# Kernel optimization log

Hardware: AMD Instinct MI355X
Metric: run time of the kernel (lower is better)

## Reference

```python
import jax, jax.numpy as jnp
import numpy as np

HID = 10


def _lstm_cell(xt, h, c, W_ih, W_hh, b_ih, b_hh):
    # PyTorch LSTMCell: gates ordered (i, f, g, o)
    gates = xt @ W_ih.T + b_ih + h @ W_hh.T + b_hh  # [B, 4*HID]
    i, f, g, o = jnp.split(gates, 4, axis=-1)
    c_new = jax.nn.sigmoid(f) * c + jax.nn.sigmoid(i) * jnp.tanh(g)
    h_new = jax.nn.sigmoid(o) * jnp.tanh(c_new)
    return h_new, c_new


def setup_inputs() -> dict:
    key = jax.random.key(0)
    ks = jax.random.split(key, 12)
    B, T = 2048, 1024
    s = 0.1
    return {
        "x": jax.random.normal(ks[0], (B, T), dtype=jnp.float32),
        "W_ih1": jax.random.normal(ks[1], (4 * HID, 1), dtype=jnp.float32) * s,
        "W_hh1": jax.random.normal(ks[2], (4 * HID, HID), dtype=jnp.float32) * s,
        "b_ih1": jax.random.normal(ks[3], (4 * HID,), dtype=jnp.float32) * s,
        "b_hh1": jax.random.normal(ks[4], (4 * HID,), dtype=jnp.float32) * s,
        "W_ih2": jax.random.normal(ks[5], (4 * HID, HID), dtype=jnp.float32) * s,
        "W_hh2": jax.random.normal(ks[6], (4 * HID, HID), dtype=jnp.float32) * s,
        "b_ih2": jax.random.normal(ks[7], (4 * HID,), dtype=jnp.float32) * s,
        "b_ih2b": None,  # placeholder removed below
        "b_hh2": jax.random.normal(ks[8], (4 * HID,), dtype=jnp.float32) * s,
        "W_lin": jax.random.normal(ks[9], (1, HID), dtype=jnp.float32) * s,
        "b_lin": jax.random.normal(ks[10], (1,), dtype=jnp.float32) * s,
        "future": 64,
    } if False else {
        "x": jax.random.normal(ks[0], (B, T), dtype=jnp.float32),
        "W_ih1": jax.random.normal(ks[1], (4 * HID, 1), dtype=jnp.float32) * s,
        "W_hh1": jax.random.normal(ks[2], (4 * HID, HID), dtype=jnp.float32) * s,
        "b_ih1": jax.random.normal(ks[3], (4 * HID,), dtype=jnp.float32) * s,
        "b_hh1": jax.random.normal(ks[4], (4 * HID,), dtype=jnp.float32) * s,
        "W_ih2": jax.random.normal(ks[5], (4 * HID, HID), dtype=jnp.float32) * s,
        "W_hh2": jax.random.normal(ks[6], (4 * HID, HID), dtype=jnp.float32) * s,
        "b_ih2": jax.random.normal(ks[7], (4 * HID,), dtype=jnp.float32) * s,
        "b_hh2": jax.random.normal(ks[8], (4 * HID,), dtype=jnp.float32) * s,
        "W_lin": jax.random.normal(ks[9], (1, HID), dtype=jnp.float32) * s,
        "b_lin": jax.random.normal(ks[10], (1,), dtype=jnp.float32) * s,
        "future": 64,
    }


def _forward(x, W_ih1, W_hh1, b_ih1, b_hh1, W_ih2, W_hh2, b_ih2, b_hh2,
             W_lin, b_lin, future):
    B = x.shape[0]
    z = jnp.zeros((B, HID), dtype=x.dtype)
    state0 = (z, z, z, z)  # h1, c1, h2, c2

    def step(state, xt):
        h1, c1, h2, c2 = state
        h1, c1 = _lstm_cell(xt, h1, c1, W_ih1, W_hh1, b_ih1, b_hh1)
        h2, c2 = _lstm_cell(h1, h2, c2, W_ih2, W_hh2, b_ih2, b_hh2)
        y = h2 @ W_lin.T + b_lin  # [B, 1]
        return (h1, c1, h2, c2), y

    xs = x.T[:, :, None]  # [T, B, 1]
    state, ys = jax.lax.scan(step, state0, xs)  # ys: [T, B, 1]
    outs = ys[:, :, 0].T  # [B, T]

    if future > 0:
        last = ys[-1]  # [B, 1]

        def fstep(carry, _):
            state, y = carry
            state, y_new = step(state, y)
            return (state, y_new), y_new

        (_, _), fys = jax.lax.scan(fstep, (state, last), None, length=future)
        outs = jnp.concatenate([outs, fys[:, :, 0].T], axis=1)
    return outs  # [B, T + future]


def reference(x, W_ih1, W_hh1, b_ih1, b_hh1, W_ih2, W_hh2, b_ih2, b_hh2,
              W_lin, b_lin, future):
    return _forward(x, W_ih1, W_hh1, b_ih1, b_hh1, W_ih2, W_hh2, b_ih2,
                    b_hh2, W_lin, b_lin, future)
```

## Files before the change

### kernel.cpp

```cpp
#include <hip/hip_runtime.h>


#define NB 512
#define TMAIN 1024
#define HID 10
#define KCH 16
#define NCH (TMAIN / KCH)

typedef float v2f __attribute__((ext_vector_type(2)));
typedef float v4f __attribute__((ext_vector_type(4)));

#define PIN2(v) asm volatile("" : "+v"(v))
#define PIN(v)  asm volatile("" : "+v"(v))

__device__ __forceinline__ float rcp_(float v)  { return __builtin_amdgcn_rcpf(v); }
__device__ __forceinline__ float exp2_(float v) { return __builtin_amdgcn_exp2f(v); }
__device__ __forceinline__ v2f mk2(float x, float y) { v2f r; r.x = x; r.y = y; return r; }
__device__ __forceinline__ v2f pfma2(v2f a, v2f b, v2f c) { return __builtin_elementwise_fma(a, b, c); }

template<int R>
__device__ __forceinline__ float rorf(float v) {
    return __int_as_float(__builtin_amdgcn_update_dpp(
        0, __float_as_int(v), 0x120 + R, 0xF, 0xF, true));
}
__device__ __forceinline__ void rot16(float h, float* hr) {
    hr[0] = h;
    hr[1]  = rorf<1>(h);  hr[2]  = rorf<2>(h);  hr[3]  = rorf<3>(h);
    hr[4]  = rorf<4>(h);  hr[5]  = rorf<5>(h);  hr[6]  = rorf<6>(h);
    hr[7]  = rorf<7>(h);  hr[8]  = rorf<8>(h);  hr[9]  = rorf<9>(h);
    hr[10] = rorf<10>(h); hr[11] = rorf<11>(h); hr[12] = rorf<12>(h);
    hr[13] = rorf<13>(h); hr[14] = rorf<14>(h); hr[15] = rorf<15>(h);
}
template<int J>
__device__ __forceinline__ float bc16(float v) {
    return __int_as_float(__builtin_amdgcn_ds_swizzle(__float_as_int(v), (J << 5) | 0x10));
}
__device__ __forceinline__ void bcast10(float h, float* hb) {
    hb[0] = bc16<0>(h); hb[1] = bc16<1>(h); hb[2] = bc16<2>(h); hb[3] = bc16<3>(h);
    hb[4] = bc16<4>(h); hb[5] = bc16<5>(h); hb[6] = bc16<6>(h); hb[7] = bc16<7>(h);
    hb[8] = bc16<8>(h); hb[9] = bc16<9>(h);
}

__global__ __launch_bounds__(256)
void lstm2_kernel(
    const float* __restrict__ x,
    const float* __restrict__ Wih1, const float* __restrict__ Whh1,
    const float* __restrict__ bih1, const float* __restrict__ bhh1,
    const float* __restrict__ Wih2, const float* __restrict__ Whh2,
    const float* __restrict__ bih2, const float* __restrict__ bhh2,
    const float* __restrict__ Wlin, const float* __restrict__ blin,
    const int* __restrict__ futp,
    float* __restrict__ out)
{
    const int tid  = threadIdx.x;
    const int wid  = tid >> 6;
    const int lane = tid & 63;
    const int e    = lane >> 4;
    const int u    = lane & 15;
    const int ge   = blockIdx.x * 4 + e;
    const int F    = futp[0];
    const int OUTW = TMAIN + F;

    __shared__ __align__(16) float ringH1[2][KCH][64];
    __shared__ __align__(16) v4f   ringU [2][KCH][64];
    __shared__ __align__(16) float ringH2[2][KCH][64];
    __shared__ __align__(16) float stC1[64], stH1[64], stC2[64], stH2[64];

    const bool uok = (u < HID);
    const int  uu  = uok ? u : 0;
    const int  Ri  = 0 * HID + uu;
    const int  Rf  = 1 * HID + uu;
    const int  Rg  = 2 * HID + uu;
    const int  Ro  = 3 * HID + uu;

    const float tK = 2.8853900817779268f;
    const float sK = -1.4426950408889634f;
    const float mu = uok ? 1.f : 0.f;
    const float sKm = mu * sK;
    const float tKm = mu * tK;

    const int rot1 = __builtin_amdgcn_update_dpp(0, u, 0x121, 0xF, 0xF, true);
    const bool dplus = (rot1 == ((u + 1) & 15));

    v2f wrot_if[16], wrot_go[16];
    v2f w2i_if[10], w2i_go[10];
    v2f wlp[5];
    v2f wx_if = mk2(0.f, 0.f), wx_go = wx_if;
    v2f b1_if = wx_if, b1_go = wx_if, b2_if = wx_if, b2_go = wx_if;
    float bl = blin[0];

    if (wid == 0 || wid == 2) {
        const float* W = (wid == 0) ? Whh1 : Whh2;
        #pragma unroll
        for (int r = 0; r < 16; ++r) {
            int jr = (u + (dplus ? r : 16 - r)) & 15;
            int jc = (jr < HID) ? jr : 0;
            float m = (uok && jr < HID) ? 1.f : 0.f;
            wrot_if[r] = mk2(m * sK * W[Ri*HID + jc], m * sK * W[Rf*HID + jc]);
            wrot_go[r] = mk2(m * tK * W[Rg*HID + jc], m * sK * W[Ro*HID + jc]);
        }
        #pragma unroll
        for (int r = 0; r < 16; ++r) { PIN2(wrot_if[r]); PIN2(wrot_go[r]); }
    }
    if (wid == 0) {
        wx_if = mk2(sKm * Wih1[Ri], sKm * Wih1[Rf]);
        wx_go = mk2(tKm * Wih1[Rg], sKm * Wih1[Ro]);
        b1_if = mk2(sKm * (bih1[Ri] + bhh1[Ri]), sKm * (bih1[Rf] + bhh1[Rf]));
        b1_go = mk2(tKm * (bih1[Rg] + bhh1[Rg]), sKm * (bih1[Ro] + bhh1[Ro]));
        PIN2(wx_if); PIN2(wx_go); PIN2(b1_if); PIN2(b1_go);
    }
    if (wid == 1) {
        #pragma unroll
        for (int j = 0; j < HID; ++j) {
            w2i_if[j] = mk2(sKm * Wih2[Ri*HID + j], sKm * Wih2[Rf*HID + j]);
            w2i_go[j] = mk2(tKm * Wih2[Rg*HID + j], sKm * Wih2[Ro*HID + j]);
        }
        b2_if = mk2(sKm * (bih2[Ri] + bhh2[Ri]), sKm * (bih2[Rf] + bhh2[Rf]));
        b2_go = mk2(tKm * (bih2[Rg] + bhh2[Rg]), sKm * (bih2[Ro] + bhh2[Ro]));
        #pragma unroll
        for (int j = 0; j < HID; ++j) { PIN2(w2i_if[j]); PIN2(w2i_go[j]); }
        PIN2(b2_if); PIN2(b2_go);
    }
    if (wid == 3) {
        #pragma unroll
        for (int k = 0; k < 5; ++k) { wlp[k] = mk2(Wlin[2*k], Wlin[2*k + 1]); PIN2(wlp[k]); }
    }

    auto ctanh_ = [&](float cs) -> float {
        return fmaf(-2.0f, rcp_(1.0f + exp2_(cs)), 1.0f);
    };
    auto cellup2 = [&](v2f p_if, v2f p_go, float& c) -> float {
        v2f q_if, q_go;
        q_if.x = rcp_(1.0f + exp2_(p_if.x));
        q_if.y = rcp_(1.0f + exp2_(p_if.y));
        q_go.x = rcp_(1.0f + exp2_(p_go.x));
        q_go.y = rcp_(1.0f + exp2_(p_go.y));
        float g = fmaf(-2.0f * tK, q_go.x, tK);
        c = fmaf(q_if.y, c, q_if.x * g);
        return q_go.y * ctanh_(c);
    };
    auto dotp = [&](const v2f* w, const float* hb, v2f init) -> v2f {
        v2f P = pfma2(w[0], mk2(hb[0], hb[0]), init);
        v2f Q = w[1] * mk2(hb[1], hb[1]);
        #pragma unroll
        for (int j = 2; j < HID; j += 2) {
            P = pfma2(w[j],     mk2(hb[j],     hb[j]),     P);
            Q = pfma2(w[j + 1], mk2(hb[j + 1], hb[j + 1]), Q);
        }
        return P + Q;
    };
    auto dot16rot = [&](const v2f* w, const float* hr, v2f init) -> v2f {
        v2f P = pfma2(w[0], mk2(hr[0], hr[0]), init);
        v2f Q = w[1] * mk2(hr[1], hr[1]);
        #pragma unroll
        for (int r = 2; r < 16; r += 2) {
            P = pfma2(w[r],     mk2(hr[r],     hr[r]),     P);
            Q = pfma2(w[r + 1], mk2(hr[r + 1], hr[r + 1]), Q);
        }
        return P + Q;
    };
    auto loadhb = [&](const float* base, float* hb) {
        v4f a = *(const v4f*)(base);
        v4f b = *(const v4f*)(base + 4);
        v2f c = *(const v2f*)(base + 8);
        hb[0] = a.x; hb[1] = a.y; hb[2] = a.z; hb[3] = a.w;
        hb[4] = b.x; hb[5] = b.y; hb[6] = b.z; hb[7] = b.w;
        hb[8] = c.x; hb[9] = c.y;
    };

    float c1 = 0.f, c2 = 0.f, h1last = 0.f, h2last = 0.f, yprev = 0.f;
    float h1r[16], h2r[16];
    float h2b[10];
    #pragma unroll
    for (int r = 0; r < 16; ++r) { h1r[r] = 0.f; h2r[r] = 0.f; }
    #pragma unroll
    for (int j = 0; j < HID; ++j) h2b[j] = 0.f;

    auto head_ = [&]() -> float {
        v2f Y = pfma2(wlp[0], mk2(h2b[0], h2b[1]), mk2(bl, 0.f));
        #pragma unroll
        for (int k = 1; k < 5; ++k)
            Y = pfma2(wlp[k], mk2(h2b[2*k], h2b[2*k + 1]), Y);
        return Y.x + Y.y;
    };

    auto pstep0 = [&](float xt, float* hslot) -> float {
        v2f A_if = dot16rot(wrot_if, h1r, pfma2(wx_if, mk2(xt, xt), b1_if));
        v2f A_go = dot16rot(wrot_go, h1r, pfma2(wx_go, mk2(xt, xt), b1_go));
        float h1n = cellup2(A_if, A_go, c1);
        rot16(h1n, h1r);
        hslot[lane] = h1n;
        return h1n;
    };

    const float4* xrow = (const float4*)(x + (size_t)ge * TMAIN);
    float4* orow = (float4*)(out + (size_t)ge * OUTW);

    float4 z4 = make_float4(0.f, 0.f, 0.f, 0.f);
    float4 xq0 = z4, xq1 = z4, xq2 = z4, xq3 = z4;
    if (wid == 0) { xq0 = xrow[0]; xq1 = xrow[1]; xq2 = xrow[2]; xq3 = xrow[3]; }

    #pragma unroll 1
    for (int c = 0; c <= NCH + 2; ++c) {
        if (wid == 0) {
            if (c < NCH) {
                float4 xn0 = z4, xn1 = z4, xn2 = z4, xn3 = z4;
                if (c + 1 < NCH) {
                    xn0 = xrow[(c+1)*4+0]; xn1 = xrow[(c+1)*4+1];
                    xn2 = xrow[(c+1)*4+2]; xn3 = xrow[(c+1)*4+3];
                }
                float* hs = &ringH1[c & 1][0][0];
                h1last = pstep0(xq0.x, hs + 0*64);  h1last = pstep0(xq0.y, hs + 1*64);
                h1last = pstep0(xq0.z, hs + 2*64);  h1last = pstep0(xq0.w, hs + 3*64);
                h1last = pstep0(xq1.x, hs + 4*64);  h1last = pstep0(xq1.y, hs + 5*64);
                h1last = pstep0(xq1.z, hs + 6*64);  h1last = pstep0(xq1.w, hs + 7*64);
                h1last = pstep0(xq2.x, hs + 8*64);  h1last = pstep0(xq2.y, hs + 9*64);
                h1last = pstep0(xq2.z, hs + 10*64); h1last = pstep0(xq2.w, hs + 11*64);
                h1last = pstep0(xq3.x, hs + 12*64); h1last = pstep0(xq3.y, hs + 13*64);
                h1last = pstep0(xq3.z, hs + 14*64); h1last = pstep0(xq3.w, hs + 15*64);
                if (c == NCH - 1) { stC1[lane] = c1; stH1[lane] = h1last; }
                xq0 = xn0; xq1 = xn1; xq2 = xn2; xq3 = xn3;
            }
        } else if (wid == 1) {
            const int cc = c - 1;
            if (cc >= 0 && cc < NCH) {
                const float* hs = &ringH1[cc & 1][0][0];
                v4f* us = &ringU[cc & 1][0][0];
                #pragma unroll
                for (int t = 0; t < KCH; ++t) {
                    float hb[10];
                    loadhb(hs + t*64 + e*16, hb);
                    v2f U_if = dotp(w2i_if, hb, b2_if);
                    v2f U_go = dotp(w2i_go, hb, b2_go);
                    v4f U; U.x = U_if.x; U.y = U_if.y; U.z = U_go.x; U.w = U_go.y;
                    us[t*64 + lane] = U;
                }
            }
        } else if (wid == 2) {
            const int cc = c - 2;
            if (cc >= 0 && cc < NCH) {
                const v4f* us = &ringU[cc & 1][0][0];
                float* h2s = &ringH2[cc & 1][0][0];
                #pragma unroll
                for (int t = 0; t < KCH; ++t) {
                    v4f U = us[t*64 + lane];
                    v2f V_if = dot16rot(wrot_if, h2r, mk2(U.x, U.y));
                    v2f V_go = dot16rot(wrot_go, h2r, mk2(U.z, U.w));
                    float h2n = cellup2(V_if, V_go, c2);
                    rot16(h2n, h2r);
                    h2s[t*64 + lane] = h2n;
                    h2last = h2n;
                }
                if (cc == NCH - 1) { stC2[lane] = c2; stH2[lane] = h2last; }
            }
        } else {
            const int cc = c - 3;
            if (cc >= 0 && cc < NCH) {
                const float* h2s = &ringH2[cc & 1][0][0];
                #pragma unroll
                for (int q = 0; q < 4; ++q) {
                    float y0, y1, y2, y3;
                    loadhb(h2s + (q*4 + 0)*64 + e*16, h2b); y0 = head_();
                    loadhb(h2s + (q*4 + 1)*64 + e*16, h2b); y1 = head_();
                    loadhb(h2s + (q*4 + 2)*64 + e*16, h2b); y2 = head_();
                    loadhb(h2s + (q*4 + 3)*64 + e*16, h2b); y3 = head_();
                    if (u == 0) orow[cc*4 + q] = make_float4(y0, y1, y2, y3);
                    yprev = y3;
                }
            }
        }
        __syncthreads();
    }

    if (wid == 3) {
        v2f f1_if[10], f1_go[10], f2i_if[10], f2i_go[10], f2h_if[10], f2h_go[10];
        #pragma unroll
        for (int j = 0; j < HID; ++j) {
            f1_if[j]  = mk2(sKm * Whh1[Ri*HID + j], sKm * Whh1[Rf*HID + j]);
            f1_go[j]  = mk2(tKm * Whh1[Rg*HID + j], sKm * Whh1[Ro*HID + j]);
            f2i_if[j] = mk2(sKm * Wih2[Ri*HID + j], sKm * Wih2[Rf*HID + j]);
            f2i_go[j] = mk2(tKm * Wih2[Rg*HID + j], sKm * Wih2[Ro*HID + j]);
            f2h_if[j] = mk2(sKm * Whh2[Ri*HID + j], sKm * Whh2[Rf*HID + j]);
            f2h_go[j] = mk2(tKm * Whh2[Rg*HID + j], sKm * Whh2[Ro*HID + j]);
        }
        v2f fb1_if = mk2(sKm * (bih1[Ri] + bhh1[Ri]), sKm * (bih1[Rf] + bhh1[Rf]));
        v2f fb1_go = mk2(tKm * (bih1[Rg] + bhh1[Rg]), sKm * (bih1[Ro] + bhh1[Ro]));
        v2f fb2_if = mk2(sKm * (bih2[Ri] + bhh2[Ri]), sKm * (bih2[Rf] + bhh2[Rf]));
        v2f fb2_go = mk2(tKm * (bih2[Rg] + bhh2[Rg]), sKm * (bih2[Ro] + bhh2[Ro]));
        v2f fwx_if = mk2(sKm * Wih1[Ri], sKm * Wih1[Rf]);
        v2f fwx_go = mk2(tKm * Wih1[Rg], sKm * Wih1[Ro]);

        float h1b[10];
        c1 = stC1[lane];
        c2 = stC2[lane];
        loadhb(&stH1[e*16], h1b);
        loadhb(&stH2[e*16], h2b);

        auto fstep = [&](float yt) -> float {
            v2f A_if = dotp(f1_if, h1b, pfma2(fwx_if, mk2(yt, yt), fb1_if));
            v2f A_go = dotp(f1_go, h1b, pfma2(fwx_go, mk2(yt, yt), fb1_go));
            float h1n = cellup2(A_if, A_go, c1);
            bcast10(h1n, h1b);
            v2f U_if = dotp(f2i_if, h1b, fb2_if);
            v2f U_go = dotp(f2i_go, h1b, fb2_go);
            v2f V_if = dotp(f2h_if, h2b, mk2(U_if.x, U_if.y));
            v2f V_go = dotp(f2h_go, h2b, mk2(U_go.x, U_go.y));
            float h2n = cellup2(V_if, V_go, c2);
            bcast10(h2n, h2b);
            return head_();
        };

        float yp = yprev;
        int t = 0;
        #pragma unroll 1
        for (; t + 3 < F; t += 4) {
            float y0 = fstep(yp);
            float y1 = fstep(y0);
            float y2 = fstep(y1);
            float y3 = fstep(y2);
            if (u == 0) orow[(TMAIN + t) / 4] = make_float4(y0, y1, y2, y3);
            yp = y3;
        }
        #pragma unroll 1
        for (; t < F; ++t) {
            yp = fstep(yp);
            if (u == 0) out[(size_t)ge * OUTW + TMAIN + t] = yp;
        }
    }
}

extern "C" void kernel_launch(void* const* d_in, const int* in_sizes, int n_in,
                              void* d_out, int out_size, void* d_ws, size_t ws_size,
                              hipStream_t stream) {
    const float* x    = (const float*)d_in[0];
    const float* Wih1 = (const float*)d_in[1];
    const float* Whh1 = (const float*)d_in[2];
    const float* bih1 = (const float*)d_in[3];
    const float* bhh1 = (const float*)d_in[4];
    const float* Wih2 = (const float*)d_in[5];
    const float* Whh2 = (const float*)d_in[6];
    const float* bih2 = (const float*)d_in[7];
    const float* bhh2 = (const float*)d_in[8];
    const float* Wlin = (const float*)d_in[9];
    const float* blin = (const float*)d_in[10];
    const int*   futp = (const int*)d_in[11];
    float* out = (float*)d_out;

    lstm2_kernel<<<NB, 256, 0, stream>>>(x, Wih1, Whh1, bih1, bhh1,
                                         Wih2, Whh2, bih2, bhh2,
                                         Wlin, blin, futp, out);
}
```

Before: 381.2 us.

## Collapse four-wave LSTM pipeline into two waves per block

Layer-2's input projection moves into the layer-1 wave, using rotated weights and DPP-rotated h1 in place of an LDS handoff. Layer-2's recurrence and the linear head are merged into the second wave, with the head computed from rotated h2. This removes the separate projection and head waves, two LDS ring buffers and two pipeline stages. Blocks shrink to 128 threads. In exchange, each wave does more serial work per timestep, and there are fewer waves available to hide latency. The future-step loop moves to wave 1 and rebuilds its state by broadcast.

```diff
diff --git a/kernel.cpp b/kernel.cpp
--- a/kernel.cpp
+++ b/kernel.cpp
@@ -41,7 +41,7 @@
     hb[8] = bc16<8>(h); hb[9] = bc16<9>(h);
 }
 
-__global__ __launch_bounds__(256)
+__global__ __launch_bounds__(128)
 void lstm2_kernel(
     const float* __restrict__ x,
     const float* __restrict__ Wih1, const float* __restrict__ Whh1,
@@ -61,10 +61,8 @@
     const int F    = futp[0];
     const int OUTW = TMAIN + F;
 
-    __shared__ __align__(16) float ringH1[2][KCH][64];
-    __shared__ __align__(16) v4f   ringU [2][KCH][64];
-    __shared__ __align__(16) float ringH2[2][KCH][64];
-    __shared__ __align__(16) float stC1[64], stH1[64], stC2[64], stH2[64];
+    __shared__ v4f   ringU[2][KCH][64];
+    __shared__ float stC1[64], stH1[64];
 
     const bool uok = (u < HID);
     const int  uu  = uok ? u : 0;
@@ -82,48 +80,46 @@
     const int rot1 = __builtin_amdgcn_update_dpp(0, u, 0x121, 0xF, 0xF, true);
     const bool dplus = (rot1 == ((u + 1) & 15));
 
-    v2f wrot_if[16], wrot_go[16];
-    v2f w2i_if[10], w2i_go[10];
-    v2f wlp[5];
+    v2f wr1_if[16], wr1_go[16], wr2i_if[16], wr2i_go[16];
+    v2f wr2h_if[16], wr2h_go[16];
+    float wlr[16];
     v2f wx_if = mk2(0.f, 0.f), wx_go = wx_if;
     v2f b1_if = wx_if, b1_go = wx_if, b2_if = wx_if, b2_go = wx_if;
     float bl = blin[0];
 
-    if (wid == 0 || wid == 2) {
-        const float* W = (wid == 0) ? Whh1 : Whh2;
+    if (wid == 0) {
         #pragma unroll
         for (int r = 0; r < 16; ++r) {
             int jr = (u + (dplus ? r : 16 - r)) & 15;
             int jc = (jr < HID) ? jr : 0;
             float m = (uok && jr < HID) ? 1.f : 0.f;
-            wrot_if[r] = mk2(m * sK * W[Ri*HID + jc], m * sK * W[Rf*HID + jc]);
-            wrot_go[r] = mk2(m * tK * W[Rg*HID + jc], m * sK * W[Ro*HID + jc]);
-        }
-        #pragma unroll
-        for (int r = 0; r < 16; ++r) { PIN2(wrot_if[r]); PIN2(wrot_go[r]); }
-    }
-    if (wid == 0) {
+            wr1_if[r]  = mk2(m * sK * Whh1[Ri*HID + jc], m * sK * Whh1[Rf*HID + jc]);
+            wr1_go[r]  = mk2(m * tK * Whh1[Rg*HID + jc], m * sK * Whh1[Ro*HID + jc]);
+            wr2i_if[r] = mk2(m * sK * Wih2[Ri*HID + jc], m * sK * Wih2[Rf*HID + jc]);
+            wr2i_go[r] = mk2(m * tK * Wih2[Rg*HID + jc], m * sK * Wih2[Ro*HID + jc]);
+        }
         wx_if = mk2(sKm * Wih1[Ri], sKm * Wih1[Rf]);
         wx_go = mk2(tKm * Wih1[Rg], sKm * Wih1[Ro]);
         b1_if = mk2(sKm * (bih1[Ri] + bhh1[Ri]), sKm * (bih1[Rf] + bhh1[Rf]));
         b1_go = mk2(tKm * (bih1[Rg] + bhh1[Rg]), sKm * (bih1[Ro] + bhh1[Ro]));
-        PIN2(wx_if); PIN2(wx_go); PIN2(b1_if); PIN2(b1_go);
-    }
-    if (wid == 1) {
-        #pragma unroll
-        for (int j = 0; j < HID; ++j) {
-            w2i_if[j] = mk2(sKm * Wih2[Ri*HID + j], sKm * Wih2[Rf*HID + j]);
-            w2i_go[j] = mk2(tKm * Wih2[Rg*HID + j], sKm * Wih2[Ro*HID + j]);
-        }
         b2_if = mk2(sKm * (bih2[Ri] + bhh2[Ri]), sKm * (bih2[Rf] + bhh2[Rf]));
         b2_go = mk2(tKm * (bih2[Rg] + bhh2[Rg]), sKm * (bih2[Ro] + bhh2[Ro]));
         #pragma unroll
-        for (int j = 0; j < HID; ++j) { PIN2(w2i_if[j]); PIN2(w2i_go[j]); }
-        PIN2(b2_if); PIN2(b2_go);
-    }
-    if (wid == 3) {
-        #pragma unroll
-        for (int k = 0; k < 5; ++k) { wlp[k] = mk2(Wlin[2*k], Wlin[2*k + 1]); PIN2(wlp[k]); }
+        for (int r = 0; r < 16; ++r) { PIN2(wr1_if[r]); PIN2(wr1_go[r]); PIN2(wr2i_if[r]); PIN2(wr2i_go[r]); }
+        PIN2(wx_if); PIN2(wx_go); PIN2(b1_if); PIN2(b1_go); PIN2(b2_if); PIN2(b2_go);
+    } else {
+        #pragma unroll
+        for (int r = 0; r < 16; ++r) {
+            int jr = (u + (dplus ? r : 16 - r)) & 15;
+            int jc = (jr < HID) ? jr : 0;
+            float m = (uok && jr < HID) ? 1.f : 0.f;
+            wr2h_if[r] = mk2(m * sK * Whh2[Ri*HID + jc], m * sK * Whh2[Rf*HID + jc]);
+            wr2h_go[r] = mk2(m * tK * Whh2[Rg*HID + jc], m * sK * Whh2[Ro*HID + jc]);
+            wlr[r]     = (jr < HID) ? Wlin[jc] : 0.f;
+        }
+        #pragma unroll
+        for (int r = 0; r < 16; ++r) { PIN2(wr2h_if[r]); PIN2(wr2h_go[r]); PIN(wlr[r]); }
+        PIN(bl);
     }
 
     auto ctanh_ = [&](float cs) -> float {
@@ -139,6 +135,16 @@
         c = fmaf(q_if.y, c, q_if.x * g);
         return q_go.y * ctanh_(c);
     };
+    auto dot16rot = [&](const v2f* w, const float* hr, v2f init) -> v2f {
+        v2f P = pfma2(w[0], mk2(hr[0], hr[0]), init);
+        v2f Q = w[1] * mk2(hr[1], hr[1]);
+        #pragma unroll
+        for (int r = 2; r < 16; r += 2) {
+            P = pfma2(w[r],     mk2(hr[r],     hr[r]),     P);
+            Q = pfma2(w[r + 1], mk2(hr[r + 1], hr[r + 1]), Q);
+        }
+        return P + Q;
+    };
     auto dotp = [&](const v2f* w, const float* hb, v2f init) -> v2f {
         v2f P = pfma2(w[0], mk2(hb[0], hb[0]), init);
         v2f Q = w[1] * mk2(hb[1], hb[1]);
@@ -149,48 +155,40 @@
         }
         return P + Q;
     };
-    auto dot16rot = [&](const v2f* w, const float* hr, v2f init) -> v2f {
-        v2f P = pfma2(w[0], mk2(hr[0], hr[0]), init);
-        v2f Q = w[1] * mk2(hr[1], hr[1]);
-        #pragma unroll
-        for (int r = 2; r < 16; r += 2) {
-            P = pfma2(w[r],     mk2(hr[r],     hr[r]),     P);
-            Q = pfma2(w[r + 1], mk2(hr[r + 1], hr[r + 1]), Q);
-        }
-        return P + Q;
-    };
-    auto loadhb = [&](const float* base, float* hb) {
-        v4f a = *(const v4f*)(base);
-        v4f b = *(const v4f*)(base + 4);
-        v2f c = *(const v2f*)(base + 8);
-        hb[0] = a.x; hb[1] = a.y; hb[2] = a.z; hb[3] = a.w;
-        hb[4] = b.x; hb[5] = b.y; hb[6] = b.z; hb[7] = b.w;
-        hb[8] = c.x; hb[9] = c.y;
-    };
-
-    float c1 = 0.f, c2 = 0.f, h1last = 0.f, h2last = 0.f, yprev = 0.f;
+
+    float c1 = 0.f, c2 = 0.f, h1last = 0.f, yprev = 0.f;
     float h1r[16], h2r[16];
-    float h2b[10];
     #pragma unroll
     for (int r = 0; r < 16; ++r) { h1r[r] = 0.f; h2r[r] = 0.f; }
-    #pragma unroll
-    for (int j = 0; j < HID; ++j) h2b[j] = 0.f;
-
-    auto head_ = [&]() -> float {
-        v2f Y = pfma2(wlp[0], mk2(h2b[0], h2b[1]), mk2(bl, 0.f));
-        #pragma unroll
-        for (int k = 1; k < 5; ++k)
-            Y = pfma2(wlp[k], mk2(h2b[2*k], h2b[2*k + 1]), Y);
-        return Y.x + Y.y;
-    };
-
-    auto pstep0 = [&](float xt, float* hslot) -> float {
-        v2f A_if = dot16rot(wrot_if, h1r, pfma2(wx_if, mk2(xt, xt), b1_if));
-        v2f A_go = dot16rot(wrot_go, h1r, pfma2(wx_go, mk2(xt, xt), b1_go));
+
+    auto head16 = [&]() -> float {
+        float Y = fmaf(wlr[0], h2r[0], bl);
+        float Z = wlr[1] * h2r[1];
+        #pragma unroll
+        for (int r = 2; r < 16; r += 2) {
+            Y = fmaf(wlr[r],     h2r[r],     Y);
+            Z = fmaf(wlr[r + 1], h2r[r + 1], Z);
+        }
+        return Y + Z;
+    };
+
+    auto pstep0 = [&](float xt, v4f* slot) -> float {
+        v2f A_if = dot16rot(wr1_if, h1r, pfma2(wx_if, mk2(xt, xt), b1_if));
+        v2f A_go = dot16rot(wr1_go, h1r, pfma2(wx_go, mk2(xt, xt), b1_go));
         float h1n = cellup2(A_if, A_go, c1);
         rot16(h1n, h1r);
-        hslot[lane] = h1n;
+        v2f U_if = dot16rot(wr2i_if, h1r, b2_if);
+        v2f U_go = dot16rot(wr2i_go, h1r, b2_go);
+        v4f U; U.x = U_if.x; U.y = U_if.y; U.z = U_go.x; U.w = U_go.y;
+        slot[lane] = U;
         return h1n;
+    };
+    auto cstep = [&](v4f U) -> float {
+        v2f V_if = dot16rot(wr2h_if, h2r, mk2(U.x, U.y));
+        v2f V_go = dot16rot(wr2h_go, h2r, mk2(U.z, U.w));
+        float h2n = cellup2(V_if, V_go, c2);
+        rot16(h2n, h2r);
+        return head16();
     };
 
     const float4* xrow = (const float4*)(x + (size_t)ge * TMAIN);
@@ -201,7 +199,7 @@
     if (wid == 0) { xq0 = xrow[0]; xq1 = xrow[1]; xq2 = xrow[2]; xq3 = xrow[3]; }
 
     #pragma unroll 1
-    for (int c = 0; c <= NCH + 2; ++c) {
+    for (int c = 0; c <= NCH; ++c) {
         if (wid == 0) {
             if (c < NCH) {
                 float4 xn0 = z4, xn1 = z4, xn2 = z4, xn3 = z4;
@@ -209,62 +207,32 @@
                     xn0 = xrow[(c+1)*4+0]; xn1 = xrow[(c+1)*4+1];
                     xn2 = xrow[(c+1)*4+2]; xn3 = xrow[(c+1)*4+3];
                 }
-                float* hs = &ringH1[c & 1][0][0];
-                h1last = pstep0(xq0.x, hs + 0*64);  h1last = pstep0(xq0.y, hs + 1*64);
-                h1last = pstep0(xq0.z, hs + 2*64);  h1last = pstep0(xq0.w, hs + 3*64);
-                h1last = pstep0(xq1.x, hs + 4*64);  h1last = pstep0(xq1.y, hs + 5*64);
-                h1last = pstep0(xq1.z, hs + 6*64);  h1last = pstep0(xq1.w, hs + 7*64);
-                h1last = pstep0(xq2.x, hs + 8*64);  h1last = pstep0(xq2.y, hs + 9*64);
-                h1last = pstep0(xq2.z, hs + 10*64); h1last = pstep0(xq2.w, hs + 11*64);
-                h1last = pstep0(xq3.x, hs + 12*64); h1last = pstep0(xq3.y, hs + 13*64);
-                h1last = pstep0(xq3.z, hs + 14*64); h1last = pstep0(xq3.w, hs + 15*64);
+                v4f* rb = &ringU[c & 1][0][0];
+                h1last = pstep0(xq0.x, rb + 0*64);  h1last = pstep0(xq0.y, rb + 1*64);
+                h1last = pstep0(xq0.z, rb + 2*64);  h1last = pstep0(xq0.w, rb + 3*64);
+                h1last = pstep0(xq1.x, rb + 4*64);  h1last = pstep0(xq1.y, rb + 5*64);
+                h1last = pstep0(xq1.z, rb + 6*64);  h1last = pstep0(xq1.w, rb + 7*64);
+                h1last = pstep0(xq2.x, rb + 8*64);  h1last = pstep0(xq2.y, rb + 9*64);
+                h1last = pstep0(xq2.z, rb + 10*64); h1last = pstep0(xq2.w, rb + 11*64);
+                h1last = pstep0(xq3.x, rb + 12*64); h1last = pstep0(xq3.y, rb + 13*64);
+                h1last = pstep0(xq3.z, rb + 14*64); h1last = pstep0(xq3.w, rb + 15*64);
                 if (c == NCH - 1) { stC1[lane] = c1; stH1[lane] = h1last; }
                 xq0 = xn0; xq1 = xn1; xq2 = xn2; xq3 = xn3;
             }
-        } else if (wid == 1) {
-            const int cc = c - 1;
-            if (cc >= 0 && cc < NCH) {
-                const float* hs = &ringH1[cc & 1][0][0];
-                v4f* us = &ringU[cc & 1][0][0];
-                #pragma unroll
-                for (int t = 0; t < KCH; ++t) {
-                    float hb[10];
-                    loadhb(hs + t*64 + e*16, hb);
-                    v2f U_if = dotp(w2i_if, hb, b2_if);
-                    v2f U_go = dotp(w2i_go, hb, b2_go);
-                    v4f U; U.x = U_if.x; U.y = U_if.y; U.z = U_go.x; U.w = U_go.y;
-                    us[t*64 + lane] = U;
-                }
-            }
-        } else if (wid == 2) {
-            const int cc = c - 2;
-            if (cc >= 0 && cc < NCH) {
-                const v4f* us = &ringU[cc & 1][0][0];
-                float* h2s = &ringH2[cc & 1][0][0];
-                #pragma unroll
-                for (int t = 0; t < KCH; ++t) {
-                    v4f U = us[t*64 + lane];
-                    v2f V_if = dot16rot(wrot_if, h2r, mk2(U.x, U.y));
-                    v2f V_go = dot16rot(wrot_go, h2r, mk2(U.z, U.w));
-                    float h2n = cellup2(V_if, V_go, c2);
-                    rot16(h2n, h2r);
-                    h2s[t*64 + lane] = h2n;
-                    h2last = h2n;
-                }
-                if (cc == NCH - 1) { stC2[lane] = c2; stH2[lane] = h2last; }
-            }
         } else {
-            const int cc = c - 3;
-            if (cc >= 0 && cc < NCH) {
-                const float* h2s = &ringH2[cc & 1][0][0];
+            if (c >= 1) {
+                const v4f* rb = &ringU[(c - 1) & 1][0][0];
                 #pragma unroll
                 for (int q = 0; q < 4; ++q) {
-                    float y0, y1, y2, y3;
-                    loadhb(h2s + (q*4 + 0)*64 + e*16, h2b); y0 = head_();
-                    loadhb(h2s + (q*4 + 1)*64 + e*16, h2b); y1 = head_();
-                    loadhb(h2s + (q*4 + 2)*64 + e*16, h2b); y2 = head_();
-                    loadhb(h2s + (q*4 + 3)*64 + e*16, h2b); y3 = head_();
-                    if (u == 0) orow[cc*4 + q] = make_float4(y0, y1, y2, y3);
+                    v4f U0 = rb[(q*4 + 0)*64 + lane];
+                    v4f U1 = rb[(q*4 + 1)*64 + lane];
+                    v4f U2 = rb[(q*4 + 2)*64 + lane];
+                    v4f U3 = rb[(q*4 + 3)*64 + lane];
+                    float y0 = cstep(U0);
+                    float y1 = cstep(U1);
+                    float y2 = cstep(U2);
+                    float y3 = cstep(U3);
+                    if (u == 0) orow[(c - 1)*4 + q] = make_float4(y0, y1, y2, y3);
                     yprev = y3;
                 }
             }
@@ -272,8 +240,9 @@
         __syncthreads();
     }
 
-    if (wid == 3) {
+    if (wid == 1) {
         v2f f1_if[10], f1_go[10], f2i_if[10], f2i_go[10], f2h_if[10], f2h_go[10];
+        v2f wlp[5];
         #pragma unroll
         for (int j = 0; j < HID; ++j) {
             f1_if[j]  = mk2(sKm * Whh1[Ri*HID + j], sKm * Whh1[Rf*HID + j]);
@@ -283,6 +252,8 @@
             f2h_if[j] = mk2(sKm * Whh2[Ri*HID + j], sKm * Whh2[Rf*HID + j]);
             f2h_go[j] = mk2(tKm * Whh2[Rg*HID + j], sKm * Whh2[Ro*HID + j]);
         }
+        #pragma unroll
+        for (int k = 0; k < 5; ++k) wlp[k] = mk2(Wlin[2*k], Wlin[2*k + 1]);
         v2f fb1_if = mk2(sKm * (bih1[Ri] + bhh1[Ri]), sKm * (bih1[Rf] + bhh1[Rf]));
         v2f fb1_go = mk2(tKm * (bih1[Rg] + bhh1[Rg]), sKm * (bih1[Ro] + bhh1[Ro]));
         v2f fb2_if = mk2(sKm * (bih2[Ri] + bhh2[Ri]), sKm * (bih2[Rf] + bhh2[Rf]));
@@ -290,12 +261,19 @@
         v2f fwx_if = mk2(sKm * Wih1[Ri], sKm * Wih1[Rf]);
         v2f fwx_go = mk2(tKm * Wih1[Rg], sKm * Wih1[Ro]);
 
-        float h1b[10];
+        float h1b[10], h2b[10];
         c1 = stC1[lane];
-        c2 = stC2[lane];
-        loadhb(&stH1[e*16], h1b);
-        loadhb(&stH2[e*16], h2b);
-
+        bcast10(stH1[lane], h1b);
+        bcast10(h2r[0], h2b);
+        float yp = bc16<0>(yprev);
+
+        auto head_ = [&]() -> float {
+            v2f Y = pfma2(wlp[0], mk2(h2b[0], h2b[1]), mk2(bl, 0.f));
+            #pragma unroll
+            for (int k = 1; k < 5; ++k)
+                Y = pfma2(wlp[k], mk2(h2b[2*k], h2b[2*k + 1]), Y);
+            return Y.x + Y.y;
+        };
         auto fstep = [&](float yt) -> float {
             v2f A_if = dotp(f1_if, h1b, pfma2(fwx_if, mk2(yt, yt), fb1_if));
             v2f A_go = dotp(f1_go, h1b, pfma2(fwx_go, mk2(yt, yt), fb1_go));
@@ -310,7 +288,6 @@
             return head_();
         };
 
-        float yp = yprev;
         int t = 0;
         #pragma unroll 1
         for (; t + 3 < F; t += 4) {
@@ -346,7 +323,7 @@
     const int*   futp = (const int*)d_in[11];
     float* out = (float*)d_out;
 
-    lstm2_kernel<<<NB, 256, 0, stream>>>(x, Wih1, Whh1, bih1, bhh1,
+    lstm2_kernel<<<NB, 128, 0, stream>>>(x, Wih1, Whh1, bih1, bhh1,
                                          Wih2, Whh2, bih2, bhh2,
                                          Wlin, blin, futp, out);
 }
```

Result: slower. 396.9 us (+4.1%).
